# Performance work log

Hardware: AMD Instinct MI355X
Metric: run time of the kernel (lower is better)

The kernel has to match this reference:

```python
import jax, jax.numpy as jnp
import numpy as np

B, S, D_MODEL, D_INT = 4, 2048, 1024, 512
ALPHA = 0.3


def setup_inputs() -> dict:
    key = jax.random.key(0)
    ks = jax.random.split(key, 8)
    scale = 1.0 / np.sqrt(D_MODEL)
    inp = {
        "z_real": jax.random.normal(ks[0], (B, S, D_MODEL), dtype=jnp.float32),
        "z_imag": jax.random.normal(ks[1], (B, S, D_MODEL), dtype=jnp.float32),
        "Wq_r": jax.random.normal(ks[2], (D_MODEL, D_INT), dtype=jnp.float32) * scale,
        "Wq_i": jax.random.normal(ks[3], (D_MODEL, D_INT), dtype=jnp.float32) * scale,
        "Wk_r": jax.random.normal(ks[4], (D_MODEL, D_INT), dtype=jnp.float32) * scale,
        "Wk_i": jax.random.normal(ks[5], (D_MODEL, D_INT), dtype=jnp.float32) * scale,
        "Wv_r": jax.random.normal(ks[6], (D_MODEL, D_INT), dtype=jnp.float32) * scale,
        "Wv_i": jax.random.normal(ks[7], (D_MODEL, D_INT), dtype=jnp.float32) * scale,
    }
    return inp


def _complex_proj(zr, zi, Wr, Wi):
    # (zr + i*zi) @ (Wr + i*Wi) computed via 4 real matmuls, as in the torch code
    out_r = zr @ Wr - zi @ Wi
    out_i = zi @ Wr + zr @ Wi
    return out_r + 1j * out_i  # complex64


def reference(z_real, z_imag, Wq_r, Wq_i, Wk_r, Wk_i, Wv_r, Wv_i):
    q = _complex_proj(z_real, z_imag, Wq_r, Wq_i)  # [B,S,D_INT] complex64
    k = _complex_proj(z_real, z_imag, Wk_r, Wk_i)
    v = _complex_proj(z_real, z_imag, Wv_r, Wv_i)

    # attn_scores = q @ k^H : [B,S,S] complex64
    attn_scores = jnp.einsum("bsd,btd->bst", q, jnp.conj(k))

    # variant == 'hybrid': (|scores| + alpha*cos(angle(scores))) / sqrt(d_k)
    mag = jnp.abs(attn_scores)
    phase = jnp.cos(jnp.angle(attn_scores))
    scores = (mag + ALPHA * phase) / np.sqrt(D_INT)

    attn_weights = jax.nn.softmax(scores, axis=-1)  # [B,S,S] float32
    output = jnp.einsum("bst,btd->bsd", attn_weights.astype(jnp.complex64), v)
    return output, attn_weights
```

## Files before the change

kernel.cpp:

```cpp
#include <hip/hip_runtime.h>
#include <hip/hip_bf16.h>

typedef unsigned short u16;
typedef u16   u16x4 __attribute__((ext_vector_type(4)));
typedef u16   u16x8 __attribute__((ext_vector_type(8)));
typedef short v8s   __attribute__((ext_vector_type(8)));
typedef float fx4   __attribute__((ext_vector_type(4)));

#define DEVINL __device__ __forceinline__

DEVINL u16 f2bf(float x){
    unsigned u = __float_as_uint(x);
    u = u + 0x7FFFu + ((u >> 16) & 1u);
    return (u16)(u >> 16);
}
DEVINL float bf2f(u16 h){ return __uint_as_float(((unsigned)h) << 16); }

DEVINL void gload16(const u16* g, u16* l){
    __builtin_amdgcn_global_load_lds(
        (const __attribute__((address_space(1))) void*)g,
        (__attribute__((address_space(3))) void*)l, 16, 0, 0);
}

__global__ void convZ_kernel(const float* __restrict__ zr, const float* __restrict__ zi,
                             u16* __restrict__ Zh, u16* __restrict__ Zl){
    int idx = blockIdx.x * blockDim.x + threadIdx.x;
    size_t i4 = (size_t)idx * 4;
    int m = (int)(i4 >> 11);
    int c = (int)(i4 & 2047);
    const float* src = (c < 1024) ? (zr + (size_t)m*1024 + c)
                                  : (zi + (size_t)m*1024 + (c - 1024));
    fx4 v = *(const fx4*)src;
    u16x4 h, l;
#pragma unroll
    for (int j = 0; j < 4; j++){
        u16 hh = f2bf(v[j]); h[j] = hh; l[j] = f2bf(v[j] - bf2f(hh));
    }
    *(u16x4*)(Zh + i4) = h;
    *(u16x4*)(Zl + i4) = l;
}

__global__ void convW_kernel(const float* __restrict__ Wq_r, const float* __restrict__ Wq_i,
                             const float* __restrict__ Wk_r, const float* __restrict__ Wk_i,
                             const float* __restrict__ Wv_r, const float* __restrict__ Wv_i,
                             u16* __restrict__ Wth, u16* __restrict__ Wtl){
    __shared__ float t[32][33];
    int k0 = blockIdx.x * 32;
    int c0 = blockIdx.y * 32;
    int blk = c0 >> 9;  int j0 = c0 & 511;
    int pair = blk >> 1, ri = blk & 1;
    int hh = k0 >> 10;  int ks0 = k0 & 1023;
    const float* Ws[6] = {Wq_r, Wq_i, Wk_r, Wk_i, Wv_r, Wv_i};
    const float* src; float sign = 1.f;
    if (ri == 0){ if (hh == 0) src = Ws[pair*2]; else { src = Ws[pair*2+1]; sign = -1.f; } }
    else        { src = (hh == 0) ? Ws[pair*2+1] : Ws[pair*2]; }
    int tx = threadIdx.x, ty = threadIdx.y;
    for (int yy = ty; yy < 32; yy += 8)
        t[yy][tx] = src[(size_t)(ks0 + yy)*512 + j0 + tx];
    __syncthreads();
    for (int yy = ty; yy < 32; yy += 8){
        float v = sign * t[tx][yy];
        u16 h2 = f2bf(v);
        size_t o = (size_t)(c0 + yy)*2048 + k0 + tx;
        Wth[o] = h2;
        Wtl[o] = f2bf(v - bf2f(h2));
    }
}

__global__ void q2_kernel(const u16* __restrict__ Chi, const u16* __restrict__ Clo,
                          u16* __restrict__ Q2h, u16* __restrict__ Q2l){
    int idx = blockIdx.x * blockDim.x + threadIdx.x;
    size_t i4 = (size_t)idx * 4;
    int m = (int)(i4 >> 10); int j = (int)(i4 & 1023);
    size_t soff; u16 x;
    if (j < 512){ soff = (size_t)m*3072 + 512 + j; x = 0; }
    else        { soff = (size_t)m*3072 + (j - 512); x = 0x8000; }
    u16x4 h = *(const u16x4*)(Chi + soff);
    u16x4 l = *(const u16x4*)(Clo + soff);
#pragma unroll
    for (int q = 0; q < 4; q++){ h[q] = (u16)(h[q] ^ x); l[q] = (u16)(l[q] ^ x); }
    *(u16x4*)(Q2h + i4) = h;
    *(u16x4*)(Q2l + i4) = l;
}

__global__ void vt_kernel(const u16* __restrict__ C, int colOff, u16* __restrict__ Vt){
    __shared__ u16 t[32][34];
    int t0 = blockIdx.x * 32; int d0 = blockIdx.y * 32; int b = blockIdx.z;
    int tx = threadIdx.x, ty = threadIdx.y;
    const u16* src = C + (size_t)b*2048*3072 + colOff;
    for (int yy = ty; yy < 32; yy += 8)
        t[yy][tx] = src[(size_t)(t0 + yy)*3072 + d0 + tx];
    __syncthreads();
    u16* dst = Vt + (size_t)b*512*2048;
    for (int yy = ty; yy < 32; yy += 8)
        dst[(size_t)(d0 + yy)*2048 + t0 + tx] = t[tx][yy];
}

__global__ __launch_bounds__(256)
void softmax_kernel(float* __restrict__ H, const float* __restrict__ SiP, u16* __restrict__ Wbf){
    int row = blockIdx.x;
    float* p = H + (size_t)row * 2048;
    const float* q = SiP + (size_t)row * 2048;
    int tid = threadIdx.x;
    fx4 v[2];
#pragma unroll
    for (int i = 0; i < 2; i++){
        fx4 sr = *(fx4*)(p + i*1024 + tid*4);
        fx4 si = *(const fx4*)(q + i*1024 + tid*4);
#pragma unroll
        for (int j = 0; j < 4; j++){
            float mag = sqrtf(sr[j]*sr[j] + si[j]*si[j]);
            float ph  = sr[j] / fmaxf(mag, 1e-30f);
            v[i][j] = (mag + 0.3f*ph) * 0.044194173824159216f;
        }
    }
    float m = -1e30f;
#pragma unroll
    for (int i = 0; i < 2; i++)
#pragma unroll
        for (int j = 0; j < 4; j++) m = fmaxf(m, v[i][j]);
    for (int k = 1; k < 64; k <<= 1) m = fmaxf(m, __shfl_xor(m, k));
    __shared__ float sm[4], ss[4];
    int w = tid >> 6, lane = tid & 63;
    if (lane == 0) sm[w] = m;
    __syncthreads();
    m = fmaxf(fmaxf(sm[0], sm[1]), fmaxf(sm[2], sm[3]));
    float s = 0.f;
#pragma unroll
    for (int i = 0; i < 2; i++)
#pragma unroll
        for (int j = 0; j < 4; j++){ v[i][j] = __expf(v[i][j] - m); s += v[i][j]; }
    for (int k = 1; k < 64; k <<= 1) s += __shfl_xor(s, k);
    if (lane == 0) ss[w] = s;
    __syncthreads();
    s = ss[0] + ss[1] + ss[2] + ss[3];
    float inv = 1.f / s;
    u16* wb = Wbf + (size_t)row * 2048;
#pragma unroll
    for (int i = 0; i < 2; i++){
        fx4 o; u16x4 ob;
#pragma unroll
        for (int j = 0; j < 4; j++){ o[j] = v[i][j] * inv; ob[j] = f2bf(o[j]); }
        *(fx4*)(p + i*1024 + tid*4) = o;
        *(u16x4*)(wb + i*1024 + tid*4) = ob;
    }
}

template<int SPLIT, int EPI>
__global__ __launch_bounds__(256, 2)
void gemm_bt(const u16* __restrict__ Ah, const u16* __restrict__ Al,
             long long aBatch, int lda,
             const u16* __restrict__ Bh, const u16* __restrict__ Bl,
             long long bBatch, int ldb,
             float* __restrict__ Cf, u16* __restrict__ Ch, u16* __restrict__ Cl,
             long long cBatch, int ldc, int ostride, int nk)
{
    constexpr int NT = SPLIT ? 4 : 2;
    __shared__ u16 smem[NT * 8192];

    int z = blockIdx.z;
    const u16* Ab  = Ah + (size_t)(aBatch * z) + (size_t)blockIdx.y * 128 * lda;
    const u16* Bb  = Bh + (size_t)(bBatch * z) + (size_t)blockIdx.x * 128 * ldb;

    int tid = threadIdx.x;
    int lane = tid & 63, w = tid >> 6;
    int wm = w & 1, wn = w >> 1;
    int frow = lane & 15, g = lane >> 4;

    int srow = w * 32 + (lane >> 3);
    int slog = (lane & 7) ^ (lane >> 3);
    const u16* pA  = Ab + (size_t)srow * lda + slog * 8;
    const u16* pB  = Bb + (size_t)srow * ldb + slog * 8;
    const u16* pAl = nullptr; const u16* pBl = nullptr;
    if constexpr (SPLIT){
        pAl = Al + (size_t)(aBatch * z) + (size_t)blockIdx.y * 128 * lda + (size_t)srow * lda + slog * 8;
        pBl = Bl + (size_t)(bBatch * z) + (size_t)blockIdx.x * 128 * ldb + (size_t)srow * ldb + slog * 8;
    }
    u16* ldsA  = smem + w * 2048;
    u16* ldsB  = smem + 8192 + w * 2048;
    u16* ldsAl = smem + 16384 + w * 2048;
    u16* ldsBl = smem + 24576 + w * 2048;

    fx4 acc[4][4] = {};

    for (int kt = 0; kt < nk; ++kt){
#pragma unroll
        for (int c = 0; c < 4; c++){
            size_t ga = (size_t)c * 8 * lda;
            size_t gb = (size_t)c * 8 * ldb;
            gload16(pA + ga, ldsA + c * 512);
            gload16(pB + gb, ldsB + c * 512);
            if constexpr (SPLIT){
                gload16(pAl + ga, ldsAl + c * 512);
                gload16(pBl + gb, ldsBl + c * 512);
            }
        }
        __syncthreads();

#pragma unroll
        for (int s = 0; s < 2; s++){
            int ko = ((g + 4*s) ^ (frow & 7)) * 8;
            v8s a_h[4], b_h[4];
#pragma unroll
            for (int mi = 0; mi < 4; mi++)
                a_h[mi] = *(const v8s*)(smem + (wm*64 + mi*16 + frow)*64 + ko);
#pragma unroll
            for (int ni = 0; ni < 4; ni++)
                b_h[ni] = *(const v8s*)(smem + 8192 + (wn*64 + ni*16 + frow)*64 + ko);
            if constexpr (SPLIT){
                v8s a_l[4], b_l[4];
#pragma unroll
                for (int mi = 0; mi < 4; mi++)
                    a_l[mi] = *(const v8s*)(smem + 16384 + (wm*64 + mi*16 + frow)*64 + ko);
#pragma unroll
                for (int ni = 0; ni < 4; ni++)
                    b_l[ni] = *(const v8s*)(smem + 24576 + (wn*64 + ni*16 + frow)*64 + ko);
#pragma unroll
                for (int mi = 0; mi < 4; mi++)
#pragma unroll
                    for (int ni = 0; ni < 4; ni++){
                        acc[mi][ni] = __builtin_amdgcn_mfma_f32_16x16x32_bf16(a_h[mi], b_h[ni], acc[mi][ni], 0, 0, 0);
                        acc[mi][ni] = __builtin_amdgcn_mfma_f32_16x16x32_bf16(a_h[mi], b_l[ni], acc[mi][ni], 0, 0, 0);
                        acc[mi][ni] = __builtin_amdgcn_mfma_f32_16x16x32_bf16(a_l[mi], b_h[ni], acc[mi][ni], 0, 0, 0);
                    }
            } else {
#pragma unroll
                for (int mi = 0; mi < 4; mi++)
#pragma unroll
                    for (int ni = 0; ni < 4; ni++)
                        acc[mi][ni] = __builtin_amdgcn_mfma_f32_16x16x32_bf16(a_h[mi], b_h[ni], acc[mi][ni], 0, 0, 0);
            }
        }
        __syncthreads();
        pA += 64; pB += 64;
        if constexpr (SPLIT){ pAl += 64; pBl += 64; }
    }

    int gcol0 = blockIdx.x * 128 + wn * 64;
    int grow0 = blockIdx.y * 128 + wm * 64;
    int rgrp  = (lane >> 4) * 4;
    if constexpr (EPI == 0){
        float* Cb = Cf + (size_t)(cBatch * z);
#pragma unroll
        for (int mi = 0; mi < 4; mi++)
#pragma unroll
            for (int ni = 0; ni < 4; ni++){
                int col = gcol0 + ni*16 + frow;
#pragma unroll
                for (int r = 0; r < 4; r++){
                    int row = grow0 + mi*16 + rgrp + r;
                    Cb[((size_t)row * ldc + col) * (size_t)ostride] = acc[mi][ni][r];
                }
            }
    } else {
        u16* Chb = Ch + (size_t)(cBatch * z);
        u16* Clb = Cl + (size_t)(cBatch * z);
#pragma unroll
        for (int mi = 0; mi < 4; mi++)
#pragma unroll
            for (int ni = 0; ni < 4; ni++){
                int col = gcol0 + ni*16 + frow;
#pragma unroll
                for (int r = 0; r < 4; r++){
                    int row = grow0 + mi*16 + rgrp + r;
                    float v = acc[mi][ni][r];
                    u16 hh = f2bf(v);
                    size_t o = (size_t)row * ldc + col;
                    Chb[o] = hh;
                    Clb[o] = f2bf(v - bf2f(hh));
                }
            }
    }
}

extern "C" void kernel_launch(void* const* d_in, const int* in_sizes, int n_in,
                              void* d_out, int out_size, void* d_ws, size_t ws_size,
                              hipStream_t stream)
{
    const float* zr   = (const float*)d_in[0];
    const float* zi   = (const float*)d_in[1];
    const float* Wq_r = (const float*)d_in[2];
    const float* Wq_i = (const float*)d_in[3];
    const float* Wk_r = (const float*)d_in[4];
    const float* Wk_i = (const float*)d_in[5];
    const float* Wv_r = (const float*)d_in[6];
    const float* Wv_i = (const float*)d_in[7];

    constexpr long long Bn = 4, S = 2048, DI = 512;
    char* ws = (char*)d_ws;
    u16* Chi = (u16*)ws;
    u16* Clo = Chi + 25165824;
    u16* Q2h = Clo + 25165824;
    u16* Q2l = Q2h + 8388608;
    char* ws2 = ws + 134217728;
    u16* Zh  = (u16*)ws2;
    u16* Zl  = Zh + 16777216;
    u16* Wth = Zl + 16777216;
    u16* Wtl = Wth + 6291456;
    float* Si = (float*)ws2;
    u16* Vt  = (u16*)(ws2 + 67108864);
    u16* Vti = Vt + 4194304;
    u16* Wbf = (u16*)ws;

    long long attn_elems = Bn * S * S;
    bool interleaved = ((long long)out_size - attn_elems) == 2LL * Bn * S * DI;
    float* outP = (float*)d_out;
    float* attn = outP + ((long long)out_size - attn_elems);

    dim3 b256(256);
    convZ_kernel<<<16384, b256, 0, stream>>>(zr, zi, Zh, Zl);
    convW_kernel<<<dim3(64, 96), dim3(32, 8), 0, stream>>>(Wq_r, Wq_i, Wk_r, Wk_i, Wv_r, Wv_i, Wth, Wtl);

    gemm_bt<1,1><<<dim3(24, 64, 1), b256, 0, stream>>>(
        Zh, Zl, 0, 2048,
        Wth, Wtl, 0, 2048,
        nullptr, Chi, Clo, 0, 3072, 1, 2048/64);

    q2_kernel<<<8192, b256, 0, stream>>>(Chi, Clo, Q2h, Q2l);

    gemm_bt<1,0><<<dim3(16, 16, 4), b256, 0, stream>>>(
        Chi, Clo, 2048LL*3072, 3072,
        Chi + 1024, Clo + 1024, 2048LL*3072, 3072,
        attn, nullptr, nullptr, 2048LL*2048, 2048, 1, 1024/64);

    gemm_bt<1,0><<<dim3(16, 16, 4), b256, 0, stream>>>(
        Q2h, Q2l, 2048LL*1024, 1024,
        Chi + 1024, Clo + 1024, 2048LL*3072, 3072,
        Si, nullptr, nullptr, 2048LL*2048, 2048, 1, 1024/64);

    vt_kernel<<<dim3(64, 16, 4), dim3(32, 8), 0, stream>>>(Chi, 2048, Vt);
    if (interleaved)
        vt_kernel<<<dim3(64, 16, 4), dim3(32, 8), 0, stream>>>(Chi, 2560, Vti);

    softmax_kernel<<<8192, b256, 0, stream>>>(attn, Si, Wbf);

    if (!interleaved){
        gemm_bt<0,0><<<dim3(4, 16, 4), b256, 0, stream>>>(
            Wbf, nullptr, 2048LL*2048, 2048,
            Vt, nullptr, 512LL*2048, 2048,
            outP, nullptr, nullptr, 2048LL*512, 512, 1, 2048/64);
    } else {
        gemm_bt<0,0><<<dim3(4, 16, 4), b256, 0, stream>>>(
            Wbf, nullptr, 2048LL*2048, 2048,
            Vt, nullptr, 512LL*2048, 2048,
            outP, nullptr, nullptr, 2048LL*512*2, 512, 2, 2048/64);
        gemm_bt<0,0><<<dim3(4, 16, 4), b256, 0, stream>>>(
            Wbf, nullptr, 2048LL*2048, 2048,
            Vti, nullptr, 512LL*2048, 2048,
            outP + 1, nullptr, nullptr, 2048LL*512*2, 512, 2, 2048/64);
    }
    (void)in_sizes; (void)n_in; (void)ws_size;
}
```

Baseline: 714.7 us.

## Use Gauss three-multiply trick for complex attention score GEMMs

Replaces the two K=1024 real GEMMs for the complex score product with three K=512 GEMMs (qr·kr, qi·ki, and (qr+qi)·(kr−ki)). A prep kernel builds the summed/differenced split-bf16 operands, and new epilogues accumulate into the existing float buffers. This cuts matrix-core work by about a quarter but adds extra read-modify-write passes over the large score buffers. It also introduces cancellation that may affect accuracy.

```diff
diff --git a/kernel.cpp b/kernel.cpp
--- a/kernel.cpp
+++ b/kernel.cpp
@@ -67,20 +67,27 @@
     }
 }
 
-__global__ void q2_kernel(const u16* __restrict__ Chi, const u16* __restrict__ Clo,
-                          u16* __restrict__ Q2h, u16* __restrict__ Q2l){
+__global__ void prep_kernel(const u16* __restrict__ Chi, const u16* __restrict__ Clo,
+                            u16* __restrict__ qsh, u16* __restrict__ qsl,
+                            u16* __restrict__ kdh, u16* __restrict__ kdl){
     int idx = blockIdx.x * blockDim.x + threadIdx.x;
     size_t i4 = (size_t)idx * 4;
-    int m = (int)(i4 >> 10); int j = (int)(i4 & 1023);
-    size_t soff; u16 x;
-    if (j < 512){ soff = (size_t)m*3072 + 512 + j; x = 0; }
-    else        { soff = (size_t)m*3072 + (j - 512); x = 0x8000; }
-    u16x4 h = *(const u16x4*)(Chi + soff);
-    u16x4 l = *(const u16x4*)(Clo + soff);
-#pragma unroll
-    for (int q = 0; q < 4; q++){ h[q] = (u16)(h[q] ^ x); l[q] = (u16)(l[q] ^ x); }
-    *(u16x4*)(Q2h + i4) = h;
-    *(u16x4*)(Q2l + i4) = l;
+    int m = (int)(i4 >> 9); int c = (int)(i4 & 511);
+    size_t base = (size_t)m * 3072 + c;
+    u16x4 qrh = *(const u16x4*)(Chi + base),        qrl = *(const u16x4*)(Clo + base);
+    u16x4 qih = *(const u16x4*)(Chi + base + 512),  qil = *(const u16x4*)(Clo + base + 512);
+    u16x4 krh = *(const u16x4*)(Chi + base + 1024), krl = *(const u16x4*)(Clo + base + 1024);
+    u16x4 kih = *(const u16x4*)(Chi + base + 1536), kil = *(const u16x4*)(Clo + base + 1536);
+    u16x4 oqh, oql, okh, okl;
+#pragma unroll
+    for (int j = 0; j < 4; j++){
+        float qs = (bf2f(qrh[j]) + bf2f(qrl[j])) + (bf2f(qih[j]) + bf2f(qil[j]));
+        float kd = (bf2f(krh[j]) + bf2f(krl[j])) - (bf2f(kih[j]) + bf2f(kil[j]));
+        u16 h1 = f2bf(qs); oqh[j] = h1; oql[j] = f2bf(qs - bf2f(h1));
+        u16 h2 = f2bf(kd); okh[j] = h2; okl[j] = f2bf(kd - bf2f(h2));
+    }
+    *(u16x4*)(qsh + i4) = oqh;  *(u16x4*)(qsl + i4) = oql;
+    *(u16x4*)(kdh + i4) = okh;  *(u16x4*)(kdl + i4) = okl;
 }
 
 __global__ void vt_kernel(const u16* __restrict__ C, int colOff, u16* __restrict__ Vt){
@@ -152,7 +159,8 @@
              long long aBatch, int lda,
              const u16* __restrict__ Bh, const u16* __restrict__ Bl,
              long long bBatch, int ldb,
-             float* __restrict__ Cf, u16* __restrict__ Ch, u16* __restrict__ Cl,
+             float* __restrict__ Cf, float* __restrict__ Cg,
+             u16* __restrict__ Ch, u16* __restrict__ Cl,
              long long cBatch, int ldc, int ostride, int nk)
 {
     constexpr int NT = SPLIT ? 4 : 2;
@@ -239,8 +247,9 @@
     int gcol0 = blockIdx.x * 128 + wn * 64;
     int grow0 = blockIdx.y * 128 + wm * 64;
     int rgrp  = (lane >> 4) * 4;
-    if constexpr (EPI == 0){
+    if constexpr (EPI == 0 || EPI == 2 || EPI == 3){
         float* Cb = Cf + (size_t)(cBatch * z);
+        float* Gb = (EPI == 3) ? Cg + (size_t)(cBatch * z) : nullptr;
 #pragma unroll
         for (int mi = 0; mi < 4; mi++)
 #pragma unroll
@@ -249,7 +258,17 @@
 #pragma unroll
                 for (int r = 0; r < 4; r++){
                     int row = grow0 + mi*16 + rgrp + r;
-                    Cb[((size_t)row * ldc + col) * (size_t)ostride] = acc[mi][ni][r];
+                    size_t o = ((size_t)row * ldc + col);
+                    float a = acc[mi][ni][r];
+                    if constexpr (EPI == 0){
+                        Cb[o * (size_t)ostride] = a;
+                    } else if constexpr (EPI == 2){
+                        Cb[o] += a;
+                    } else {
+                        float c0 = Cb[o];
+                        Cb[o] = c0 + a;
+                        Gb[o] = a - c0;
+                    }
                 }
             }
     } else {
@@ -290,16 +309,18 @@
     char* ws = (char*)d_ws;
     u16* Chi = (u16*)ws;
     u16* Clo = Chi + 25165824;
-    u16* Q2h = Clo + 25165824;
-    u16* Q2l = Q2h + 8388608;
+    u16* qsh = (u16*)(ws + 100663296);
+    u16* qsl = qsh + 4194304;
+    u16* kdh = qsl + 4194304;
+    u16* kdl = kdh + 4194304;
+    u16* Vt  = qsh;
+    u16* Vti = qsh + 4194304;
     char* ws2 = ws + 134217728;
     u16* Zh  = (u16*)ws2;
     u16* Zl  = Zh + 16777216;
     u16* Wth = Zl + 16777216;
     u16* Wtl = Wth + 6291456;
-    float* Si = (float*)ws2;
-    u16* Vt  = (u16*)(ws2 + 67108864);
-    u16* Vti = Vt + 4194304;
+    float* bufX = (float*)ws2;
     u16* Wbf = (u16*)ws;
 
     long long attn_elems = Bn * S * S;
@@ -314,40 +335,45 @@
     gemm_bt<1,1><<<dim3(24, 64, 1), b256, 0, stream>>>(
         Zh, Zl, 0, 2048,
         Wth, Wtl, 0, 2048,
-        nullptr, Chi, Clo, 0, 3072, 1, 2048/64);
-
-    q2_kernel<<<8192, b256, 0, stream>>>(Chi, Clo, Q2h, Q2l);
+        nullptr, nullptr, Chi, Clo, 0, 3072, 1, 2048/64);
+
+    prep_kernel<<<4096, b256, 0, stream>>>(Chi, Clo, qsh, qsl, kdh, kdl);
 
     gemm_bt<1,0><<<dim3(16, 16, 4), b256, 0, stream>>>(
         Chi, Clo, 2048LL*3072, 3072,
         Chi + 1024, Clo + 1024, 2048LL*3072, 3072,
-        attn, nullptr, nullptr, 2048LL*2048, 2048, 1, 1024/64);
-
-    gemm_bt<1,0><<<dim3(16, 16, 4), b256, 0, stream>>>(
-        Q2h, Q2l, 2048LL*1024, 1024,
-        Chi + 1024, Clo + 1024, 2048LL*3072, 3072,
-        Si, nullptr, nullptr, 2048LL*2048, 2048, 1, 1024/64);
+        attn, nullptr, nullptr, nullptr, 2048LL*2048, 2048, 1, 512/64);
+
+    gemm_bt<1,3><<<dim3(16, 16, 4), b256, 0, stream>>>(
+        Chi + 512, Clo + 512, 2048LL*3072, 3072,
+        Chi + 1536, Clo + 1536, 2048LL*3072, 3072,
+        attn, bufX, nullptr, nullptr, 2048LL*2048, 2048, 1, 512/64);
+
+    gemm_bt<1,2><<<dim3(16, 16, 4), b256, 0, stream>>>(
+        qsh, qsl, 2048LL*512, 512,
+        kdh, kdl, 2048LL*512, 512,
+        bufX, nullptr, nullptr, nullptr, 2048LL*2048, 2048, 1, 512/64);
 
     vt_kernel<<<dim3(64, 16, 4), dim3(32, 8), 0, stream>>>(Chi, 2048, Vt);
     if (interleaved)
         vt_kernel<<<dim3(64, 16, 4), dim3(32, 8), 0, stream>>>(Chi, 2560, Vti);
 
-    softmax_kernel<<<8192, b256, 0, stream>>>(attn, Si, Wbf);
+    softmax_kernel<<<8192, b256, 0, stream>>>(attn, bufX, Wbf);
 
     if (!interleaved){
         gemm_bt<0,0><<<dim3(4, 16, 4), b256, 0, stream>>>(
             Wbf, nullptr, 2048LL*2048, 2048,
             Vt, nullptr, 512LL*2048, 2048,
-            outP, nullptr, nullptr, 2048LL*512, 512, 1, 2048/64);
+            outP, nullptr, nullptr, nullptr, 2048LL*512, 512, 1, 2048/64);
     } else {
         gemm_bt<0,0><<<dim3(4, 16, 4), b256, 0, stream>>>(
             Wbf, nullptr, 2048LL*2048, 2048,
             Vt, nullptr, 512LL*2048, 2048,
-            outP, nullptr, nullptr, 2048LL*512*2, 512, 2, 2048/64);
+            outP, nullptr, nullptr, nullptr, 2048LL*512*2, 512, 2, 2048/64);
         gemm_bt<0,0><<<dim3(4, 16, 4), b256, 0, stream>>>(
             Wbf, nullptr, 2048LL*2048, 2048,
             Vti, nullptr, 512LL*2048, 2048,
-            outP + 1, nullptr, nullptr, 2048LL*512*2, 512, 2, 2048/64);
+            outP + 1, nullptr, nullptr, nullptr, 2048LL*512*2, 512, 2, 2048/64);
     }
     (void)in_sizes; (void)n_in; (void)ws_size;
 }
```

After: 729.2 us. +2.0%, slower.

## Fuse real and imaginary score GEMMs into one complex-score kernel

Applied to the files above, without the earlier changes.

Replaces the q2 sign/permute kernel and two separate split-bf16 score GEMMs with a single kernel that loads Q and K real/imag hi/lo tiles once and accumulates both the real and imaginary parts of q·conj(k) using MFMA. The imaginary sign flip is done in registers by XORing the sign bit. This removes one pass over Q/K operand loads, the Q2 buffer traffic and one launch. In exchange the new kernel holds twice the accumulators, which raises register pressure, and it has no double buffering and writes its outputs with scalar, uncoalesced stores.

```diff
diff --git a/kernel.cpp b/kernel.cpp
--- a/kernel.cpp
+++ b/kernel.cpp
@@ -67,22 +67,6 @@
     }
 }
 
-__global__ void q2_kernel(const u16* __restrict__ Chi, const u16* __restrict__ Clo,
-                          u16* __restrict__ Q2h, u16* __restrict__ Q2l){
-    int idx = blockIdx.x * blockDim.x + threadIdx.x;
-    size_t i4 = (size_t)idx * 4;
-    int m = (int)(i4 >> 10); int j = (int)(i4 & 1023);
-    size_t soff; u16 x;
-    if (j < 512){ soff = (size_t)m*3072 + 512 + j; x = 0; }
-    else        { soff = (size_t)m*3072 + (j - 512); x = 0x8000; }
-    u16x4 h = *(const u16x4*)(Chi + soff);
-    u16x4 l = *(const u16x4*)(Clo + soff);
-#pragma unroll
-    for (int q = 0; q < 4; q++){ h[q] = (u16)(h[q] ^ x); l[q] = (u16)(l[q] ^ x); }
-    *(u16x4*)(Q2h + i4) = h;
-    *(u16x4*)(Q2l + i4) = l;
-}
-
 __global__ void vt_kernel(const u16* __restrict__ C, int colOff, u16* __restrict__ Vt){
     __shared__ u16 t[32][34];
     int t0 = blockIdx.x * 32; int d0 = blockIdx.y * 32; int b = blockIdx.z;
@@ -144,6 +128,101 @@
         *(fx4*)(p + i*1024 + tid*4) = o;
         *(u16x4*)(wb + i*1024 + tid*4) = ob;
     }
+}
+
+__global__ __launch_bounds__(256, 2)
+void score2_kernel(const u16* __restrict__ Chi, const u16* __restrict__ Clo,
+                   float* __restrict__ Sr, float* __restrict__ Si)
+{
+    __shared__ u16 smem[8 * 4096];
+    int z = blockIdx.z;
+    int tid = threadIdx.x, lane = tid & 63, w = tid >> 6;
+    int wm = w & 1, wn = w >> 1;
+    int frow = lane & 15, g = lane >> 4;
+
+    int srow = w * 32 + (lane >> 2);
+    int scol = (lane & 3) * 8;
+    size_t qoff = ((size_t)z*2048 + blockIdx.y*128 + srow) * 3072 + scol;
+    size_t koff = ((size_t)z*2048 + blockIdx.x*128 + srow) * 3072 + 1024 + scol;
+    u16* L = smem;
+
+    v8s sgn8;
+#pragma unroll
+    for (int j = 0; j < 8; j++) sgn8[j] = (short)0x8000;
+
+    fx4 aR[4][4] = {}, aI[4][4] = {};
+
+    for (int kt = 0; kt < 16; ++kt){
+        int k0 = kt * 32;
+#pragma unroll
+        for (int c = 0; c < 2; c++){
+            size_t q = qoff + (size_t)c * 49152 + k0;
+            size_t k = koff + (size_t)c * 49152 + k0;
+            u16* d = L + w * 1024 + c * 512;
+            gload16(Chi + q,       d);
+            gload16(Clo + q,       d + 4096);
+            gload16(Chi + q + 512, d + 8192);
+            gload16(Clo + q + 512, d + 12288);
+            gload16(Chi + k,       d + 16384);
+            gload16(Clo + k,       d + 20480);
+            gload16(Chi + k + 512, d + 24576);
+            gload16(Clo + k + 512, d + 28672);
+        }
+        __syncthreads();
+
+        v8s ar_h[4], ar_l[4], ai_h[4], ai_l[4];
+#pragma unroll
+        for (int mi = 0; mi < 4; mi++){
+            int off = (wm*64 + mi*16 + frow) * 32 + g * 8;
+            ar_h[mi] = *(const v8s*)(L + off);
+            ar_l[mi] = *(const v8s*)(L + 4096  + off);
+            ai_h[mi] = *(const v8s*)(L + 8192  + off);
+            ai_l[mi] = *(const v8s*)(L + 12288 + off);
+        }
+#pragma unroll
+        for (int ni = 0; ni < 4; ni++){
+            int off = (wn*64 + ni*16 + frow) * 32 + g * 8;
+            v8s br_h = *(const v8s*)(L + 16384 + off);
+            v8s br_l = *(const v8s*)(L + 20480 + off);
+            v8s bi_h = *(const v8s*)(L + 24576 + off);
+            v8s bi_l = *(const v8s*)(L + 28672 + off);
+            v8s bn_h = bi_h ^ sgn8;
+            v8s bn_l = bi_l ^ sgn8;
+#pragma unroll
+            for (int mi = 0; mi < 4; mi++){
+                aR[mi][ni] = __builtin_amdgcn_mfma_f32_16x16x32_bf16(ar_h[mi], br_h, aR[mi][ni], 0, 0, 0);
+                aR[mi][ni] = __builtin_amdgcn_mfma_f32_16x16x32_bf16(ar_h[mi], br_l, aR[mi][ni], 0, 0, 0);
+                aR[mi][ni] = __builtin_amdgcn_mfma_f32_16x16x32_bf16(ar_l[mi], br_h, aR[mi][ni], 0, 0, 0);
+                aR[mi][ni] = __builtin_amdgcn_mfma_f32_16x16x32_bf16(ai_h[mi], bi_h, aR[mi][ni], 0, 0, 0);
+                aR[mi][ni] = __builtin_amdgcn_mfma_f32_16x16x32_bf16(ai_h[mi], bi_l, aR[mi][ni], 0, 0, 0);
+                aR[mi][ni] = __builtin_amdgcn_mfma_f32_16x16x32_bf16(ai_l[mi], bi_h, aR[mi][ni], 0, 0, 0);
+                aI[mi][ni] = __builtin_amdgcn_mfma_f32_16x16x32_bf16(ai_h[mi], br_h, aI[mi][ni], 0, 0, 0);
+                aI[mi][ni] = __builtin_amdgcn_mfma_f32_16x16x32_bf16(ai_h[mi], br_l, aI[mi][ni], 0, 0, 0);
+                aI[mi][ni] = __builtin_amdgcn_mfma_f32_16x16x32_bf16(ai_l[mi], br_h, aI[mi][ni], 0, 0, 0);
+                aI[mi][ni] = __builtin_amdgcn_mfma_f32_16x16x32_bf16(ar_h[mi], bn_h, aI[mi][ni], 0, 0, 0);
+                aI[mi][ni] = __builtin_amdgcn_mfma_f32_16x16x32_bf16(ar_h[mi], bn_l, aI[mi][ni], 0, 0, 0);
+                aI[mi][ni] = __builtin_amdgcn_mfma_f32_16x16x32_bf16(ar_l[mi], bn_h, aI[mi][ni], 0, 0, 0);
+            }
+        }
+        __syncthreads();
+    }
+
+    size_t cb = (size_t)z * 2048 * 2048;
+    int gcol0 = blockIdx.x * 128 + wn * 64;
+    int grow0 = blockIdx.y * 128 + wm * 64;
+    int rgrp  = (lane >> 4) * 4;
+#pragma unroll
+    for (int mi = 0; mi < 4; mi++)
+#pragma unroll
+        for (int ni = 0; ni < 4; ni++){
+            int col = gcol0 + ni*16 + frow;
+#pragma unroll
+            for (int r = 0; r < 4; r++){
+                size_t o = cb + (size_t)(grow0 + mi*16 + rgrp + r) * 2048 + col;
+                Sr[o] = aR[mi][ni][r];
+                Si[o] = aI[mi][ni][r];
+            }
+        }
 }
 
 template<int SPLIT, int EPI>
@@ -290,14 +369,12 @@
     char* ws = (char*)d_ws;
     u16* Chi = (u16*)ws;
     u16* Clo = Chi + 25165824;
-    u16* Q2h = Clo + 25165824;
-    u16* Q2l = Q2h + 8388608;
     char* ws2 = ws + 134217728;
     u16* Zh  = (u16*)ws2;
     u16* Zl  = Zh + 16777216;
     u16* Wth = Zl + 16777216;
     u16* Wtl = Wth + 6291456;
-    float* Si = (float*)ws2;
+    float* bufX = (float*)ws2;
     u16* Vt  = (u16*)(ws2 + 67108864);
     u16* Vti = Vt + 4194304;
     u16* Wbf = (u16*)ws;
@@ -316,23 +393,13 @@
         Wth, Wtl, 0, 2048,
         nullptr, Chi, Clo, 0, 3072, 1, 2048/64);
 
-    q2_kernel<<<8192, b256, 0, stream>>>(Chi, Clo, Q2h, Q2l);
-
-    gemm_bt<1,0><<<dim3(16, 16, 4), b256, 0, stream>>>(
-        Chi, Clo, 2048LL*3072, 3072,
-        Chi + 1024, Clo + 1024, 2048LL*3072, 3072,
-        attn, nullptr, nullptr, 2048LL*2048, 2048, 1, 1024/64);
-
-    gemm_bt<1,0><<<dim3(16, 16, 4), b256, 0, stream>>>(
-        Q2h, Q2l, 2048LL*1024, 1024,
-        Chi + 1024, Clo + 1024, 2048LL*3072, 3072,
-        Si, nullptr, nullptr, 2048LL*2048, 2048, 1, 1024/64);
+    score2_kernel<<<dim3(16, 16, 4), b256, 0, stream>>>(Chi, Clo, attn, bufX);
 
     vt_kernel<<<dim3(64, 16, 4), dim3(32, 8), 0, stream>>>(Chi, 2048, Vt);
     if (interleaved)
         vt_kernel<<<dim3(64, 16, 4), dim3(32, 8), 0, stream>>>(Chi, 2560, Vti);
 
-    softmax_kernel<<<8192, b256, 0, stream>>>(attn, Si, Wbf);
+    softmax_kernel<<<8192, b256, 0, stream>>>(attn, bufX, Wbf);
 
     if (!interleaved){
         gemm_bt<0,0><<<dim3(4, 16, 4), b256, 0, stream>>>(
```

Result: faster. 672.0 us (-6.0%).
